# Kernel tuning notes

Measured on AMD Instinct MI355X. Metric: run time of the kernel, lower is better.

## Reference

```python
import jax, jax.numpy as jnp
import numpy as np

N_NODES = 50000
N_EDGES = 800000
D_IN = 256
HID = 128
OUT = 64
NEG_SLOPE = 0.2  # PyG GATConv default leaky_relu slope
EPS = 1e-16      # PyG softmax denominator epsilon


def _gat_conv(x, src, dst, W_src, W_dst, att_src, att_dst, bias, n_nodes):
    """Single-head PyG GATConv with add_self_loops=False.
    Returns (out [N, C_out], alpha [E])."""
    h_src = x @ W_src                     # [N, C]
    h_dst = x @ W_dst                     # [N, C]
    a_src = h_src @ att_src               # [N]
    a_dst = h_dst @ att_dst               # [N]
    logits = jax.nn.leaky_relu(a_src[src] + a_dst[dst], NEG_SLOPE)  # [E]
    # segment softmax over incoming edges of each dst node
    m = jax.ops.segment_max(logits, dst, num_segments=n_nodes)      # [N]
    e = jnp.exp(logits - m[dst])                                    # [E]
    denom = jax.ops.segment_sum(e, dst, num_segments=n_nodes)       # [N]
    alpha = e / (denom[dst] + EPS)                                  # [E]
    msg = h_src[src] * alpha[:, None]                               # [E, C]
    out = jax.ops.segment_sum(msg, dst, num_segments=n_nodes) + bias
    return out, alpha


def setup_inputs() -> dict:
    key = jax.random.key(0)
    ks = jax.random.split(key, 16)
    s = 0.05
    x = jax.random.normal(ks[0], (N_NODES, D_IN), dtype=jnp.float32)
    edge_index = jax.random.randint(ks[1], (2, N_EDGES), 0, N_NODES, dtype=jnp.int64)
    return {
        "x": x,
        "edge_index": edge_index,
        "W_src1": jax.random.normal(ks[2], (D_IN, HID), jnp.float32) * s,
        "W_dst1": jax.random.normal(ks[3], (D_IN, HID), jnp.float32) * s,
        "att_src1": jax.random.normal(ks[4], (HID,), jnp.float32) * s,
        "att_dst1": jax.random.normal(ks[5], (HID,), jnp.float32) * s,
        "b1": jnp.zeros((HID,), jnp.float32),
        "W_lin1": jax.random.normal(ks[6], (D_IN, HID), jnp.float32) * s,
        "b_lin1": jnp.zeros((HID,), jnp.float32),
        "W_src2": jax.random.normal(ks[7], (HID, OUT), jnp.float32) * s,
        "W_dst2": jax.random.normal(ks[8], (HID, OUT), jnp.float32) * s,
        "att_src2": jax.random.normal(ks[9], (OUT,), jnp.float32) * s,
        "att_dst2": jax.random.normal(ks[10], (OUT,), jnp.float32) * s,
        "b2": jnp.zeros((OUT,), jnp.float32),
        "W_lin2": jax.random.normal(ks[11], (HID, OUT), jnp.float32) * s,
        "b_lin2": jnp.zeros((OUT,), jnp.float32),
    }


def reference(x, edge_index, W_src1, W_dst1, att_src1, att_dst1, b1, W_lin1, b_lin1,
              W_src2, W_dst2, att_src2, att_dst2, b2, W_lin2, b_lin2):
    src, dst = edge_index[0], edge_index[1]
    n = x.shape[0]
    h, _ = _gat_conv(x, src, dst, W_src1, W_dst1, att_src1, att_dst1, b1, n)
    h = h + x @ W_lin1 + b_lin1
    h = jax.nn.relu(h)
    out, alpha = _gat_conv(h, src, dst, W_src2, W_dst2, att_src2, att_dst2, b2, n)
    out = out + h @ W_lin2 + b_lin2
    return out, alpha
```

## Files before the change

### kernel.cpp

```cpp
#include <hip/hip_runtime.h>
#include <math.h>

#define D_IN 256
#define HID 128
#define D_OUT 64
#define NEG_SLOPE 0.2f

#define NBUCK 392
#define BCAP  2560
#define P1_EPB 2048

typedef short short8 __attribute__((ext_vector_type(8)));
typedef float floatx4 __attribute__((ext_vector_type(4)));

__device__ __forceinline__ float wave_reduce_sum(float v) {
    #pragma unroll
    for (int off = 32; off > 0; off >>= 1) v += __shfl_xor(v, off, 64);
    return v;
}
__device__ __forceinline__ int wave_scan_incl_i(int v) {
    int lane = threadIdx.x & 63;
    #pragma unroll
    for (int off = 1; off < 64; off <<= 1) {
        int t = __shfl_up(v, off, 64);
        if (lane >= off) v += t;
    }
    return v;
}

__device__ __forceinline__ short f2bf(float f) {
    unsigned u = __float_as_uint(f);
    u += 0x7fffu + ((u >> 16) & 1u);
    return (short)(u >> 16);
}
__device__ __forceinline__ unsigned pk2(float a, float b) {
    return (unsigned)(unsigned short)f2bf(a) | ((unsigned)(unsigned short)f2bf(b) << 16);
}
__device__ __forceinline__ float bflo(unsigned p) { return __uint_as_float(p << 16); }
__device__ __forceinline__ float bfhi(unsigned p) { return __uint_as_float(p & 0xffff0000u); }

__global__ void prep_kernel(const float* __restrict__ Wsrc1, const float* __restrict__ att_src1,
                            const float* __restrict__ Wdst1, const float* __restrict__ att_dst1,
                            const float* __restrict__ Wsrc2, const float* __restrict__ att_src2,
                            const float* __restrict__ Wdst2, const float* __restrict__ att_dst2,
                            const float* __restrict__ b1, const float* __restrict__ b_lin1,
                            const float* __restrict__ b2, const float* __restrict__ b_lin2,
                            float* v_src1, float* v_dst1, float* v_src2, float* v_dst2,
                            float* bsum1, float* bsum2, int* bcur) {
    int t = threadIdx.x;
    if (t < D_IN) {
        float s1 = 0.f, s2 = 0.f;
        for (int c = 0; c < HID; c++) {
            s1 += Wsrc1[t * HID + c] * att_src1[c];
            s2 += Wdst1[t * HID + c] * att_dst1[c];
        }
        v_src1[t] = s1; v_dst1[t] = s2;
    }
    if (t < HID) {
        float s1 = 0.f, s2 = 0.f;
        for (int c = 0; c < D_OUT; c++) {
            s1 += Wsrc2[t * D_OUT + c] * att_src2[c];
            s2 += Wdst2[t * D_OUT + c] * att_dst2[c];
        }
        v_src2[t] = s1; v_dst2[t] = s2;
        bsum1[t] = b1[t] + b_lin1[t];
    }
    if (t < D_OUT) bsum2[t] = b2[t] + b_lin2[t];
    for (int i = t; i < NBUCK; i += 256) bcur[i] = 0;
}

__device__ void pack_body(const float* Wa, const float* Wb, short* Wp,
                          int NTG, int NH, int total, int idx) {
    if (idx >= total) return;
    int j = idx & 7;
    int lane = (idx >> 3) & 63;
    int r = idx >> 9;
    int nt = r % NTG;
    int s = r / NTG;
    int k = s * 32 + ((lane >> 4) * 8) + j;
    int cg = nt * 16 + (lane & 15);
    const float* W = (cg < NH) ? Wa : Wb;
    int col = (cg < NH) ? cg : cg - NH;
    Wp[idx] = f2bf(W[(size_t)k * NH + col]);
}

__device__ void bucket_scatter_body(const int* __restrict__ src, const int* __restrict__ dst,
                                    int E, int* bcur, unsigned* ebuf, int blk) {
    __shared__ int hist[NBUCK];
    __shared__ int gbase[NBUCK];
    int t = threadIdx.x;
    for (int i = t; i < NBUCK; i += 256) hist[i] = 0;
    __syncthreads();
    int e0 = blk * P1_EPB;
    int e1 = e0 + P1_EPB; if (e1 > E) e1 = E;
    for (int e = e0 + t; e < e1; e += 256)
        atomicAdd(&hist[dst[e] >> 7], 1);
    __syncthreads();
    for (int i = t; i < NBUCK; i += 256) {
        gbase[i] = atomicAdd(&bcur[i], hist[i]);
        hist[i] = 0;
    }
    __syncthreads();
    for (int e = e0 + t; e < e1; e += 256) {
        int d = dst[e];
        int b = d >> 7;
        int slot = atomicAdd(&hist[b], 1);
        int pos = gbase[b] + slot;
        if (pos < BCAP)
            ebuf[(size_t)b * BCAP + pos] = (unsigned)src[e] | ((unsigned)(d & 127) << 16);
    }
}

__device__ void convert_body(const float* __restrict__ X,
                             const float* __restrict__ vsrc, const float* __restrict__ vdst,
                             unsigned short* __restrict__ xb,
                             float* __restrict__ a_src, float* __restrict__ a_dst,
                             int Nn, int rb) {
    int row = rb * 4 + (threadIdx.x >> 6);
    int lane = threadIdx.x & 63;
    if (row >= Nn) return;
    float4 v = *(const float4*)(X + (size_t)row * D_IN + lane * 4);
    float4 vs = *(const float4*)(vsrc + lane * 4);
    float4 vd = *(const float4*)(vdst + lane * 4);
    float ps = v.x * vs.x + v.y * vs.y + v.z * vs.z + v.w * vs.w;
    float pd = v.x * vd.x + v.y * vd.y + v.z * vd.z + v.w * vd.w;
    ushort4 o;
    o.x = (unsigned short)f2bf(v.x); o.y = (unsigned short)f2bf(v.y);
    o.z = (unsigned short)f2bf(v.z); o.w = (unsigned short)f2bf(v.w);
    *(ushort4*)(xb + (size_t)row * D_IN + lane * 4) = o;
    ps = wave_reduce_sum(ps);
    pd = wave_reduce_sum(pd);
    if (lane == 0) { a_src[row] = ps; a_dst[row] = pd; }
}

__global__ void fused_pre(const int* __restrict__ src, const int* __restrict__ dst, int E,
                          int* bcur, unsigned* ebuf, int P1B,
                          const float* W_src1, const float* W_lin1, short* Wp1,
                          const float* W_src2, const float* W_lin2, short* Wp2,
                          const float* __restrict__ v_src1, const float* __restrict__ v_dst1,
                          float* a_src1, float* a_dst1,
                          const float* __restrict__ X, unsigned short* __restrict__ xb, int Nn) {
    int bid = blockIdx.x;
    if (bid < P1B) {
        bucket_scatter_body(src, dst, E, bcur, ebuf, bid);
    } else if (bid < P1B + 256) {
        pack_body(W_src1, W_lin1, Wp1, 16, HID, 8 * 16 * 512, (bid - P1B) * 256 + threadIdx.x);
    } else if (bid < P1B + 320) {
        pack_body(W_src2, W_lin2, Wp2, 8, D_OUT, 4 * 8 * 512, (bid - P1B - 256) * 256 + threadIdx.x);
    } else {
        convert_body(X, v_src1, v_dst1, xb, a_src1, a_dst1, Nn, bid - (P1B + 320));
    }
}

__device__ void build_csr_body(const int* __restrict__ bcur, const unsigned* __restrict__ ebuf,
                               int* __restrict__ ssrc, int* __restrict__ row_beg,
                               int* __restrict__ row_end, int Nn, int B) {
    __shared__ int cnt[128];
    __shared__ int ofs[128];
    __shared__ int wsum[2];
    int t = threadIdx.x;
    if (t < 128) cnt[t] = 0;
    __syncthreads();
    int n = bcur[B]; if (n > BCAP) n = BCAP;
    const unsigned* eb = ebuf + (size_t)B * BCAP;
    for (int i = t; i < n; i += 256)
        atomicAdd(&cnt[eb[i] >> 16], 1);
    __syncthreads();
    int base = B * BCAP;
    int v = 0, excl = 0;
    if (t < 128) {
        v = cnt[t];
        int incl = wave_scan_incl_i(v);
        if ((t & 63) == 63) wsum[t >> 6] = incl;
        excl = incl - v;
    }
    __syncthreads();
    if (t < 128) {
        if (t >= 64) excl += wsum[0];
        int node = B * 128 + t;
        if (node < Nn) { row_beg[node] = base + excl; row_end[node] = base + excl + v; }
        ofs[t] = base + excl;
    }
    __syncthreads();
    for (int i = t; i < n; i += 256) {
        unsigned r = eb[i];
        int pos = atomicAdd(&ofs[r >> 16], 1);
        ssrc[pos] = (int)(r & 0xffffu);
    }
}

template <int KS, int NT>
__device__ void gemm_body(const unsigned short* __restrict__ A,
                          const short* __restrict__ Wp,
                          const float* __restrict__ bias,
                          unsigned short* __restrict__ outb,
                          unsigned short* __restrict__ outc, int M, int bm) {
    const int K = KS * 32;
    const int NTG = 4 * NT;
    const int NH = NT * 32;
    int tid = threadIdx.x;
    int wave = tid >> 6, lane = tid & 63;
    int mr = lane & 15, quad = lane >> 4;

    floatx4 acc[4][NT];
    #pragma unroll
    for (int i = 0; i < 4; i++)
        #pragma unroll
        for (int j = 0; j < NT; j++) acc[i][j] = (floatx4){0.f, 0.f, 0.f, 0.f};

    const unsigned short* arow[4];
    #pragma unroll
    for (int tm = 0; tm < 4; tm++) {
        int gr = bm + tm * 16 + mr;
        if (gr >= M) gr = M - 1;
        arow[tm] = A + (size_t)gr * K + quad * 8;
    }
    const short* bbase = Wp + ((size_t)(wave * NT) * 64 + lane) * 8;

    #pragma unroll
    for (int s = 0; s < KS; s++) {
        short8 af[4], bf[NT];
        #pragma unroll
        for (int tm = 0; tm < 4; tm++)
            af[tm] = *(const short8*)(arow[tm] + s * 32);
        #pragma unroll
        for (int tn = 0; tn < NT; tn++)
            bf[tn] = *(const short8*)(bbase + ((size_t)s * NTG + tn) * 512);
        #pragma unroll
        for (int tn = 0; tn < NT; tn++)
            #pragma unroll
            for (int tm = 0; tm < 4; tm++)
                acc[tm][tn] = __builtin_amdgcn_mfma_f32_16x16x32_bf16(af[tm], bf[tn],
                                                                      acc[tm][tn], 0, 0, 0);
    }

    #pragma unroll
    for (int tm = 0; tm < 4; tm++) {
        #pragma unroll
        for (int tn = 0; tn < NT; tn++) {
            int cg = wave * NT * 16 + tn * 16 + mr;
            if (cg < NH) {
                #pragma unroll
                for (int r = 0; r < 4; r++) {
                    int gr = bm + tm * 16 + quad * 4 + r;
                    if (gr < M)
                        outb[(size_t)gr * NH + cg] = (unsigned short)f2bf(acc[tm][tn][r]);
                }
            } else {
                float bv = bias[cg - NH];
                #pragma unroll
                for (int r = 0; r < 4; r++) {
                    int gr = bm + tm * 16 + quad * 4 + r;
                    if (gr < M)
                        outc[(size_t)gr * NH + (cg - NH)] = (unsigned short)f2bf(acc[tm][tn][r] + bv);
                }
            }
        }
    }
}

__global__ __launch_bounds__(256, 3) void fused_g1(const unsigned short* __restrict__ xb,
                                                   const short* __restrict__ Wp1,
                                                   const float* __restrict__ bsum1,
                                                   unsigned short* __restrict__ h1b,
                                                   unsigned short* __restrict__ lin1b,
                                                   int M, int MB,
                                                   const int* __restrict__ bcur,
                                                   const unsigned* __restrict__ ebuf,
                                                   int* ssrc, int* row_beg, int* row_end, int Nn) {
    int bid = blockIdx.x;
    int c = bid >> 3, sub = bid & 7;
    int q = c / 3, r = c - q * 3;
    if (r == 2) {
        int B = q * 8 + sub;
        if (B < NBUCK)
            build_csr_body(bcur, ebuf, ssrc, row_beg, row_end, Nn, B);
    } else {
        int gb = (q * 2 + r) * 8 + sub;
        if (gb < MB)
            gemm_body<8, 4>(xb, Wp1, bsum1, h1b, lin1b, M, gb * 64);
    }
}

template <int KS, int NT>
__global__ __launch_bounds__(256, 3) void gemm_direct(const unsigned short* __restrict__ A,
                                                      const short* __restrict__ Wp,
                                                      const float* __restrict__ bias,
                                                      unsigned short* __restrict__ outb,
                                                      unsigned short* __restrict__ outc, int M) {
    gemm_body<KS, NT>(A, Wp, bias, outb, outc, M, blockIdx.x * 64);
}

__global__ void agg1_kernel(const int* __restrict__ row_beg, const int* __restrict__ row_end,
                            const int* __restrict__ ssrc,
                            const float* __restrict__ a_src, const float* __restrict__ a_dst,
                            const unsigned short* __restrict__ h1b,
                            const unsigned short* __restrict__ linb,
                            const float* __restrict__ vs2, const float* __restrict__ vd2,
                            unsigned short* __restrict__ hb,
                            float* __restrict__ a_src2, float* __restrict__ a_dst2, int Nn) {
    int node = blockIdx.x * 4 + (threadIdx.x >> 6);
    int lane = threadIdx.x & 63;
    if (node >= Nn) return;
    int beg = row_beg[node], end = row_end[node];
    float ad = a_dst[node];

    int qh = lane >> 4, cl = lane & 15;
    float acc[8] = {0.f, 0.f, 0.f, 0.f, 0.f, 0.f, 0.f, 0.f};
    float dsum = 0.f;
    const unsigned short* hcol = h1b + cl * 8;
    int j = beg + qh;
    for (; j + 4 < end; j += 8) {
        int s0 = ssrc[j], s1 = ssrc[j + 4];
        float l0 = a_src[s0] + ad; l0 = (l0 > 0.f) ? l0 : NEG_SLOPE * l0;
        float l1 = a_src[s1] + ad; l1 = (l1 > 0.f) ? l1 : NEG_SLOPE * l1;
        float w0 = __expf(l0), w1 = __expf(l1);
        uint4 p0 = *(const uint4*)(hcol + (size_t)s0 * HID);
        uint4 p1 = *(const uint4*)(hcol + (size_t)s1 * HID);
        acc[0] += w0 * bflo(p0.x); acc[1] += w0 * bfhi(p0.x);
        acc[2] += w0 * bflo(p0.y); acc[3] += w0 * bfhi(p0.y);
        acc[4] += w0 * bflo(p0.z); acc[5] += w0 * bfhi(p0.z);
        acc[6] += w0 * bflo(p0.w); acc[7] += w0 * bfhi(p0.w);
        acc[0] += w1 * bflo(p1.x); acc[1] += w1 * bfhi(p1.x);
        acc[2] += w1 * bflo(p1.y); acc[3] += w1 * bfhi(p1.y);
        acc[4] += w1 * bflo(p1.z); acc[5] += w1 * bfhi(p1.z);
        acc[6] += w1 * bflo(p1.w); acc[7] += w1 * bfhi(p1.w);
        if (cl == 0) dsum += w0 + w1;
    }
    for (; j < end; j += 4) {
        int s0 = ssrc[j];
        float l = a_src[s0] + ad; l = (l > 0.f) ? l : NEG_SLOPE * l;
        float w = __expf(l);
        uint4 p = *(const uint4*)(hcol + (size_t)s0 * HID);
        acc[0] += w * bflo(p.x); acc[1] += w * bfhi(p.x);
        acc[2] += w * bflo(p.y); acc[3] += w * bfhi(p.y);
        acc[4] += w * bflo(p.z); acc[5] += w * bfhi(p.z);
        acc[6] += w * bflo(p.w); acc[7] += w * bfhi(p.w);
        if (cl == 0) dsum += w;
    }
    #pragma unroll
    for (int i = 0; i < 8; i++) {
        acc[i] += __shfl_xor(acc[i], 16, 64);
        acc[i] += __shfl_xor(acc[i], 32, 64);
    }
    dsum = wave_reduce_sum(dsum);
    float inv = 1.f / (dsum + 1e-16f);

    int c = cl * 8;
    uint4 lb = *(const uint4*)(linb + (size_t)node * HID + c);
    float o[8];
    o[0] = fmaxf(acc[0] * inv + bflo(lb.x), 0.f);
    o[1] = fmaxf(acc[1] * inv + bfhi(lb.x), 0.f);
    o[2] = fmaxf(acc[2] * inv + bflo(lb.y), 0.f);
    o[3] = fmaxf(acc[3] * inv + bfhi(lb.y), 0.f);
    o[4] = fmaxf(acc[4] * inv + bflo(lb.z), 0.f);
    o[5] = fmaxf(acc[5] * inv + bfhi(lb.z), 0.f);
    o[6] = fmaxf(acc[6] * inv + bflo(lb.w), 0.f);
    o[7] = fmaxf(acc[7] * inv + bfhi(lb.w), 0.f);
    if (qh == 0) {
        uint4 pk;
        pk.x = pk2(o[0], o[1]); pk.y = pk2(o[2], o[3]);
        pk.z = pk2(o[4], o[5]); pk.w = pk2(o[6], o[7]);
        *(uint4*)&hb[(size_t)node * HID + c] = pk;
    }
    float ps = 0.f, pd = 0.f;
    #pragma unroll
    for (int i = 0; i < 8; i++) { ps += o[i] * vs2[c + i]; pd += o[i] * vd2[c + i]; }
    ps = wave_reduce_sum(ps) * 0.25f;
    pd = wave_reduce_sum(pd) * 0.25f;
    if (lane == 0) { a_src2[node] = ps; a_dst2[node] = pd; }
}

__global__ void agg2_kernel(const int* __restrict__ row_beg, const int* __restrict__ row_end,
                            const int* __restrict__ ssrc,
                            const float* __restrict__ a_src, const float* __restrict__ a_dst,
                            const unsigned short* __restrict__ h2b,
                            const unsigned short* __restrict__ lin2b,
                            float* __restrict__ out, float* __restrict__ sminv, int Nn) {
    int node = blockIdx.x * 4 + (threadIdx.x >> 6);
    int lane = threadIdx.x & 63;
    if (node >= Nn) return;
    int beg = row_beg[node], end = row_end[node];
    float ad = a_dst[node];

    int oh = lane >> 3, cl = lane & 7;
    float acc[8] = {0.f, 0.f, 0.f, 0.f, 0.f, 0.f, 0.f, 0.f};
    float dsum = 0.f;
    const unsigned short* hcol = h2b + cl * 8;
    int j = beg + oh;
    for (; j + 8 < end; j += 16) {
        int s0 = ssrc[j], s1 = ssrc[j + 8];
        float l0 = a_src[s0] + ad; l0 = (l0 > 0.f) ? l0 : NEG_SLOPE * l0;
        float l1 = a_src[s1] + ad; l1 = (l1 > 0.f) ? l1 : NEG_SLOPE * l1;
        float w0 = __expf(l0), w1 = __expf(l1);
        uint4 p0 = *(const uint4*)(hcol + (size_t)s0 * D_OUT);
        uint4 p1 = *(const uint4*)(hcol + (size_t)s1 * D_OUT);
        acc[0] += w0 * bflo(p0.x); acc[1] += w0 * bfhi(p0.x);
        acc[2] += w0 * bflo(p0.y); acc[3] += w0 * bfhi(p0.y);
        acc[4] += w0 * bflo(p0.z); acc[5] += w0 * bfhi(p0.z);
        acc[6] += w0 * bflo(p0.w); acc[7] += w0 * bfhi(p0.w);
        acc[0] += w1 * bflo(p1.x); acc[1] += w1 * bfhi(p1.x);
        acc[2] += w1 * bflo(p1.y); acc[3] += w1 * bfhi(p1.y);
        acc[4] += w1 * bflo(p1.z); acc[5] += w1 * bfhi(p1.z);
        acc[6] += w1 * bflo(p1.w); acc[7] += w1 * bfhi(p1.w);
        if (cl == 0) dsum += w0 + w1;
    }
    for (; j < end; j += 8) {
        int s0 = ssrc[j];
        float l = a_src[s0] + ad; l = (l > 0.f) ? l : NEG_SLOPE * l;
        float w = __expf(l);
        uint4 p = *(const uint4*)(hcol + (size_t)s0 * D_OUT);
        acc[0] += w * bflo(p.x); acc[1] += w * bfhi(p.x);
        acc[2] += w * bflo(p.y); acc[3] += w * bfhi(p.y);
        acc[4] += w * bflo(p.z); acc[5] += w * bfhi(p.z);
        acc[6] += w * bflo(p.w); acc[7] += w * bfhi(p.w);
        if (cl == 0) dsum += w;
    }
    #pragma unroll
    for (int i = 0; i < 8; i++) {
        acc[i] += __shfl_xor(acc[i], 8, 64);
        acc[i] += __shfl_xor(acc[i], 16, 64);
        acc[i] += __shfl_xor(acc[i], 32, 64);
    }
    dsum = wave_reduce_sum(dsum);
    float inv = 1.f / (dsum + 1e-16f);
    if (lane == 0) sminv[node] = inv;

    if (oh == 0) {
        int c = cl * 8;
        uint4 lb = *(const uint4*)(lin2b + (size_t)node * D_OUT + c);
        float4 oa = make_float4(acc[0] * inv + bflo(lb.x), acc[1] * inv + bfhi(lb.x),
                                acc[2] * inv + bflo(lb.y), acc[3] * inv + bfhi(lb.y));
        float4 ob = make_float4(acc[4] * inv + bflo(lb.z), acc[5] * inv + bfhi(lb.z),
                                acc[6] * inv + bflo(lb.w), acc[7] * inv + bfhi(lb.w));
        *(float4*)&out[(size_t)node * D_OUT + c] = oa;
        *(float4*)&out[(size_t)node * D_OUT + c + 4] = ob;
    }
}

__global__ void alpha_kernel(const int* __restrict__ src, const int* __restrict__ dst,
                             const float* __restrict__ a_src2, const float* __restrict__ a_dst2,
                             const float* __restrict__ sminv, float* __restrict__ alpha, int E) {
    int e = blockIdx.x * 256 + threadIdx.x;
    if (e >= E) return;
    int s = src[e], d = dst[e];
    float l = a_src2[s] + a_dst2[d];
    l = (l > 0.f) ? l : NEG_SLOPE * l;
    alpha[e] = __expf(l) * sminv[d];
}

extern "C" void kernel_launch(void* const* d_in, const int* in_sizes, int n_in,
                              void* d_out, int out_size, void* d_ws, size_t ws_size,
                              hipStream_t stream) {
    const float* x        = (const float*)d_in[0];
    const int*   ei       = (const int*)d_in[1];
    const float* W_src1   = (const float*)d_in[2];
    const float* W_dst1   = (const float*)d_in[3];
    const float* att_src1 = (const float*)d_in[4];
    const float* att_dst1 = (const float*)d_in[5];
    const float* b1       = (const float*)d_in[6];
    const float* W_lin1   = (const float*)d_in[7];
    const float* b_lin1   = (const float*)d_in[8];
    const float* W_src2   = (const float*)d_in[9];
    const float* W_dst2   = (const float*)d_in[10];
    const float* att_src2 = (const float*)d_in[11];
    const float* att_dst2 = (const float*)d_in[12];
    const float* b2       = (const float*)d_in[13];
    const float* W_lin2   = (const float*)d_in[14];
    const float* b_lin2   = (const float*)d_in[15];

    const int Nn = in_sizes[0] / D_IN;
    const int E  = in_sizes[1] / 2;
    const int* src = ei;
    const int* dst = ei + E;

    char* w = (char*)d_ws;
    auto alloc = [&](size_t bytes) { char* p = w; w += (bytes + 255) & ~(size_t)255; return p; };
    unsigned short* xb   = (unsigned short*)alloc((size_t)Nn * D_IN * 2);
    unsigned short* h1b  = (unsigned short*)alloc((size_t)Nn * HID * 2);
    unsigned short* lin1b= (unsigned short*)alloc((size_t)Nn * HID * 2);
    unsigned short* hb   = (unsigned short*)alloc((size_t)Nn * HID * 2);
    unsigned short* h2b  = (unsigned short*)alloc((size_t)Nn * D_OUT * 2);
    unsigned short* lin2b= (unsigned short*)alloc((size_t)Nn * D_OUT * 2);
    float* a_src1 = (float*)alloc((size_t)Nn * 4);
    float* a_dst1 = (float*)alloc((size_t)Nn * 4);
    float* a_src2 = (float*)alloc((size_t)Nn * 4);
    float* a_dst2 = (float*)alloc((size_t)Nn * 4);
    float* sminv  = (float*)alloc((size_t)Nn * 4);
    int*   row_beg= (int*)alloc((size_t)Nn * 4);
    int*   row_end= (int*)alloc((size_t)Nn * 4);
    int*   bcur   = (int*)alloc((size_t)NBUCK * 4);
    unsigned* ebuf= (unsigned*)alloc((size_t)NBUCK * BCAP * 4);
    int*   ssrc   = (int*)alloc((size_t)NBUCK * BCAP * 4);
    short* Wp1    = (short*)alloc((size_t)8 * 16 * 512 * 2);
    short* Wp2    = (short*)alloc((size_t)4 * 8 * 512 * 2);
    float* v_src1 = (float*)alloc(D_IN * 4);
    float* v_dst1 = (float*)alloc(D_IN * 4);
    float* v_src2 = (float*)alloc(HID * 4);
    float* v_dst2 = (float*)alloc(HID * 4);
    float* bsum1  = (float*)alloc(HID * 4);
    float* bsum2  = (float*)alloc(D_OUT * 4);

    float* out       = (float*)d_out;
    float* alpha_out = out + (size_t)Nn * D_OUT;

    prep_kernel<<<1, 256, 0, stream>>>(W_src1, att_src1, W_dst1, att_dst1,
                                       W_src2, att_src2, W_dst2, att_dst2,
                                       b1, b_lin1, b2, b_lin2,
                                       v_src1, v_dst1, v_src2, v_dst2, bsum1, bsum2, bcur);

    int P1B = (E + P1_EPB - 1) / P1_EPB;
    int ablocks = (Nn + 3) / 4;
    fused_pre<<<P1B + 320 + ablocks, 256, 0, stream>>>(src, dst, E, bcur, ebuf, P1B,
                                             W_src1, W_lin1, Wp1, W_src2, W_lin2, Wp2,
                                             v_src1, v_dst1, a_src1, a_dst1,
                                             x, xb, Nn);

    int mblocks = (Nn + 63) / 64;
    int gchunks = (mblocks + 7) / 8;
    int cchunks = (NBUCK + 7) / 8;
    int NI = (gchunks + cchunks) * 8;
    fused_g1<<<NI, 256, 0, stream>>>(xb, Wp1, bsum1, h1b, lin1b, Nn,
                                     mblocks, bcur, ebuf, ssrc, row_beg, row_end, Nn);

    agg1_kernel<<<ablocks, 256, 0, stream>>>(row_beg, row_end, ssrc, a_src1, a_dst1, h1b, lin1b,
                                             v_src2, v_dst2, hb, a_src2, a_dst2, Nn);

    gemm_direct<4, 2><<<mblocks, 256, 0, stream>>>(hb, Wp2, bsum2, h2b, lin2b, Nn);
    agg2_kernel<<<ablocks, 256, 0, stream>>>(row_beg, row_end, ssrc, a_src2, a_dst2, h2b, lin2b,
                                             out, sminv, Nn);
    int eblocks = (E + 255) / 256;
    alpha_kernel<<<eblocks, 256, 0, stream>>>(src, dst, a_src2, a_dst2, sminv, alpha_out, E);
}
```

Before: 276.9 us.

## Split aggregation kernels across feature column slices and parallelize prep kernel

The agg1 and agg2 kernels now give each node's feature columns to 4 and 2 blocks respectively. Each wave processes 16 edges in parallel with 4 lanes per 32-column slice, instead of spreading lanes over all columns. This raises edge-level parallelism and the number of blocks for the gather-heavy aggregation. The cost is recomputing edge weights, softmax denominators and index loads once per slice. Partial a_src2/a_dst2 dot products are accumulated with atomics into buffers zeroed by memsets, and prep_kernel is spread across 25 blocks with shuffle reductions.

Result: slower. 361.5 us (+30.5%).

```diff
diff --git a/kernel.cpp b/kernel.cpp
--- a/kernel.cpp
+++ b/kernel.cpp
@@ -47,26 +47,42 @@
                             const float* __restrict__ b2, const float* __restrict__ b_lin2,
                             float* v_src1, float* v_dst1, float* v_src2, float* v_dst2,
                             float* bsum1, float* bsum2, int* bcur) {
-    int t = threadIdx.x;
-    if (t < D_IN) {
+    int bid = blockIdx.x, t = threadIdx.x;
+    if (bid < 16) {
+        int r = bid * 16 + (t >> 4), sub = t & 15;
         float s1 = 0.f, s2 = 0.f;
-        for (int c = 0; c < HID; c++) {
-            s1 += Wsrc1[t * HID + c] * att_src1[c];
-            s2 += Wdst1[t * HID + c] * att_dst1[c];
+        #pragma unroll
+        for (int k = 0; k < 8; k++) {
+            int c = sub * 8 + k;
+            s1 += Wsrc1[r * HID + c] * att_src1[c];
+            s2 += Wdst1[r * HID + c] * att_dst1[c];
         }
-        v_src1[t] = s1; v_dst1[t] = s2;
-    }
-    if (t < HID) {
+        #pragma unroll
+        for (int off = 8; off > 0; off >>= 1) {
+            s1 += __shfl_xor(s1, off, 16);
+            s2 += __shfl_xor(s2, off, 16);
+        }
+        if (sub == 0) { v_src1[r] = s1; v_dst1[r] = s2; }
+    } else if (bid < 24) {
+        int r = (bid - 16) * 16 + (t >> 4), sub = t & 15;
         float s1 = 0.f, s2 = 0.f;
-        for (int c = 0; c < D_OUT; c++) {
-            s1 += Wsrc2[t * D_OUT + c] * att_src2[c];
-            s2 += Wdst2[t * D_OUT + c] * att_dst2[c];
+        #pragma unroll
+        for (int k = 0; k < 4; k++) {
+            int c = sub * 4 + k;
+            s1 += Wsrc2[r * D_OUT + c] * att_src2[c];
+            s2 += Wdst2[r * D_OUT + c] * att_dst2[c];
         }
-        v_src2[t] = s1; v_dst2[t] = s2;
-        bsum1[t] = b1[t] + b_lin1[t];
-    }
-    if (t < D_OUT) bsum2[t] = b2[t] + b_lin2[t];
-    for (int i = t; i < NBUCK; i += 256) bcur[i] = 0;
+        #pragma unroll
+        for (int off = 8; off > 0; off >>= 1) {
+            s1 += __shfl_xor(s1, off, 16);
+            s2 += __shfl_xor(s2, off, 16);
+        }
+        if (sub == 0) { v_src2[r] = s1; v_dst2[r] = s2; }
+    } else {
+        if (t < HID) bsum1[t] = b1[t] + b_lin1[t];
+        if (t < D_OUT) bsum2[t] = b2[t] + b_lin2[t];
+        for (int i = t; i < NBUCK; i += 256) bcur[i] = 0;
+    }
 }
 
 __device__ void pack_body(const float* Wa, const float* Wb, short* Wp,
@@ -299,54 +315,39 @@
                             const float* __restrict__ vs2, const float* __restrict__ vd2,
                             unsigned short* __restrict__ hb,
                             float* __restrict__ a_src2, float* __restrict__ a_dst2, int Nn) {
-    int node = blockIdx.x * 4 + (threadIdx.x >> 6);
+    int q = blockIdx.x & 3;
+    int node = (blockIdx.x >> 2) * 4 + (threadIdx.x >> 6);
     int lane = threadIdx.x & 63;
     if (node >= Nn) return;
     int beg = row_beg[node], end = row_end[node];
     float ad = a_dst[node];
 
-    int qh = lane >> 4, cl = lane & 15;
+    int eslot = lane >> 2, cg = lane & 3;
+    int c = q * 32 + cg * 8;
+    const unsigned short* hcol = h1b + c;
     float acc[8] = {0.f, 0.f, 0.f, 0.f, 0.f, 0.f, 0.f, 0.f};
     float dsum = 0.f;
-    const unsigned short* hcol = h1b + cl * 8;
-    int j = beg + qh;
-    for (; j + 4 < end; j += 8) {
-        int s0 = ssrc[j], s1 = ssrc[j + 4];
-        float l0 = a_src[s0] + ad; l0 = (l0 > 0.f) ? l0 : NEG_SLOPE * l0;
-        float l1 = a_src[s1] + ad; l1 = (l1 > 0.f) ? l1 : NEG_SLOPE * l1;
-        float w0 = __expf(l0), w1 = __expf(l1);
-        uint4 p0 = *(const uint4*)(hcol + (size_t)s0 * HID);
-        uint4 p1 = *(const uint4*)(hcol + (size_t)s1 * HID);
-        acc[0] += w0 * bflo(p0.x); acc[1] += w0 * bfhi(p0.x);
-        acc[2] += w0 * bflo(p0.y); acc[3] += w0 * bfhi(p0.y);
-        acc[4] += w0 * bflo(p0.z); acc[5] += w0 * bfhi(p0.z);
-        acc[6] += w0 * bflo(p0.w); acc[7] += w0 * bfhi(p0.w);
-        acc[0] += w1 * bflo(p1.x); acc[1] += w1 * bfhi(p1.x);
-        acc[2] += w1 * bflo(p1.y); acc[3] += w1 * bfhi(p1.y);
-        acc[4] += w1 * bflo(p1.z); acc[5] += w1 * bfhi(p1.z);
-        acc[6] += w1 * bflo(p1.w); acc[7] += w1 * bfhi(p1.w);
-        if (cl == 0) dsum += w0 + w1;
-    }
-    for (; j < end; j += 4) {
-        int s0 = ssrc[j];
-        float l = a_src[s0] + ad; l = (l > 0.f) ? l : NEG_SLOPE * l;
+    for (int j = beg + eslot; j < end; j += 16) {
+        int s = ssrc[j];
+        float l = a_src[s] + ad; l = (l > 0.f) ? l : NEG_SLOPE * l;
         float w = __expf(l);
-        uint4 p = *(const uint4*)(hcol + (size_t)s0 * HID);
+        uint4 p = *(const uint4*)(hcol + (size_t)s * HID);
         acc[0] += w * bflo(p.x); acc[1] += w * bfhi(p.x);
         acc[2] += w * bflo(p.y); acc[3] += w * bfhi(p.y);
         acc[4] += w * bflo(p.z); acc[5] += w * bfhi(p.z);
         acc[6] += w * bflo(p.w); acc[7] += w * bfhi(p.w);
-        if (cl == 0) dsum += w;
+        if (cg == 0) dsum += w;
     }
     #pragma unroll
     for (int i = 0; i < 8; i++) {
+        acc[i] += __shfl_xor(acc[i], 4, 64);
+        acc[i] += __shfl_xor(acc[i], 8, 64);
         acc[i] += __shfl_xor(acc[i], 16, 64);
         acc[i] += __shfl_xor(acc[i], 32, 64);
     }
     dsum = wave_reduce_sum(dsum);
     float inv = 1.f / (dsum + 1e-16f);
 
-    int c = cl * 8;
     uint4 lb = *(const uint4*)(linb + (size_t)node * HID + c);
     float o[8];
     o[0] = fmaxf(acc[0] * inv + bflo(lb.x), 0.f);
@@ -357,7 +358,7 @@
     o[5] = fmaxf(acc[5] * inv + bfhi(lb.z), 0.f);
     o[6] = fmaxf(acc[6] * inv + bflo(lb.w), 0.f);
     o[7] = fmaxf(acc[7] * inv + bfhi(lb.w), 0.f);
-    if (qh == 0) {
+    if (eslot == 0) {
         uint4 pk;
         pk.x = pk2(o[0], o[1]); pk.y = pk2(o[2], o[3]);
         pk.z = pk2(o[4], o[5]); pk.w = pk2(o[6], o[7]);
@@ -366,9 +367,12 @@
     float ps = 0.f, pd = 0.f;
     #pragma unroll
     for (int i = 0; i < 8; i++) { ps += o[i] * vs2[c + i]; pd += o[i] * vd2[c + i]; }
-    ps = wave_reduce_sum(ps) * 0.25f;
-    pd = wave_reduce_sum(pd) * 0.25f;
-    if (lane == 0) { a_src2[node] = ps; a_dst2[node] = pd; }
+    ps = wave_reduce_sum(ps) * 0.0625f;
+    pd = wave_reduce_sum(pd) * 0.0625f;
+    if (lane == 0) {
+        atomicAdd(&a_src2[node], ps);
+        atomicAdd(&a_dst2[node], pd);
+    }
 }
 
 __global__ void agg2_kernel(const int* __restrict__ row_beg, const int* __restrict__ row_end,
@@ -377,57 +381,41 @@
                             const unsigned short* __restrict__ h2b,
                             const unsigned short* __restrict__ lin2b,
                             float* __restrict__ out, float* __restrict__ sminv, int Nn) {
-    int node = blockIdx.x * 4 + (threadIdx.x >> 6);
+    int h = blockIdx.x & 1;
+    int node = (blockIdx.x >> 1) * 4 + (threadIdx.x >> 6);
     int lane = threadIdx.x & 63;
     if (node >= Nn) return;
     int beg = row_beg[node], end = row_end[node];
     float ad = a_dst[node];
 
-    int oh = lane >> 3, cl = lane & 7;
+    int eslot = lane >> 2, cg = lane & 3;
+    int c = h * 32 + cg * 8;
+    const unsigned short* hcol = h2b + c;
     float acc[8] = {0.f, 0.f, 0.f, 0.f, 0.f, 0.f, 0.f, 0.f};
     float dsum = 0.f;
-    const unsigned short* hcol = h2b + cl * 8;
-    int j = beg + oh;
-    for (; j + 8 < end; j += 16) {
-        int s0 = ssrc[j], s1 = ssrc[j + 8];
-        float l0 = a_src[s0] + ad; l0 = (l0 > 0.f) ? l0 : NEG_SLOPE * l0;
-        float l1 = a_src[s1] + ad; l1 = (l1 > 0.f) ? l1 : NEG_SLOPE * l1;
-        float w0 = __expf(l0), w1 = __expf(l1);
-        uint4 p0 = *(const uint4*)(hcol + (size_t)s0 * D_OUT);
-        uint4 p1 = *(const uint4*)(hcol + (size_t)s1 * D_OUT);
-        acc[0] += w0 * bflo(p0.x); acc[1] += w0 * bfhi(p0.x);
-        acc[2] += w0 * bflo(p0.y); acc[3] += w0 * bfhi(p0.y);
-        acc[4] += w0 * bflo(p0.z); acc[5] += w0 * bfhi(p0.z);
-        acc[6] += w0 * bflo(p0.w); acc[7] += w0 * bfhi(p0.w);
-        acc[0] += w1 * bflo(p1.x); acc[1] += w1 * bfhi(p1.x);
-        acc[2] += w1 * bflo(p1.y); acc[3] += w1 * bfhi(p1.y);
-        acc[4] += w1 * bflo(p1.z); acc[5] += w1 * bfhi(p1.z);
-        acc[6] += w1 * bflo(p1.w); acc[7] += w1 * bfhi(p1.w);
-        if (cl == 0) dsum += w0 + w1;
-    }
-    for (; j < end; j += 8) {
-        int s0 = ssrc[j];
-        float l = a_src[s0] + ad; l = (l > 0.f) ? l : NEG_SLOPE * l;
+    for (int j = beg + eslot; j < end; j += 16) {
+        int s = ssrc[j];
+        float l = a_src[s] + ad; l = (l > 0.f) ? l : NEG_SLOPE * l;
         float w = __expf(l);
-        uint4 p = *(const uint4*)(hcol + (size_t)s0 * D_OUT);
+        uint4 p = *(const uint4*)(hcol + (size_t)s * D_OUT);
         acc[0] += w * bflo(p.x); acc[1] += w * bfhi(p.x);
         acc[2] += w * bflo(p.y); acc[3] += w * bfhi(p.y);
         acc[4] += w * bflo(p.z); acc[5] += w * bfhi(p.z);
         acc[6] += w * bflo(p.w); acc[7] += w * bfhi(p.w);
-        if (cl == 0) dsum += w;
+        if (cg == 0) dsum += w;
     }
     #pragma unroll
     for (int i = 0; i < 8; i++) {
+        acc[i] += __shfl_xor(acc[i], 4, 64);
         acc[i] += __shfl_xor(acc[i], 8, 64);
         acc[i] += __shfl_xor(acc[i], 16, 64);
         acc[i] += __shfl_xor(acc[i], 32, 64);
     }
     dsum = wave_reduce_sum(dsum);
     float inv = 1.f / (dsum + 1e-16f);
-    if (lane == 0) sminv[node] = inv;
-
-    if (oh == 0) {
-        int c = cl * 8;
+    if (h == 0 && lane == 0) sminv[node] = inv;
+
+    if (eslot == 0) {
         uint4 lb = *(const uint4*)(lin2b + (size_t)node * D_OUT + c);
         float4 oa = make_float4(acc[0] * inv + bflo(lb.x), acc[1] * inv + bfhi(lb.x),
                                 acc[2] * inv + bflo(lb.y), acc[3] * inv + bfhi(lb.y));
@@ -504,10 +492,13 @@
     float* out       = (float*)d_out;
     float* alpha_out = out + (size_t)Nn * D_OUT;
 
-    prep_kernel<<<1, 256, 0, stream>>>(W_src1, att_src1, W_dst1, att_dst1,
-                                       W_src2, att_src2, W_dst2, att_dst2,
-                                       b1, b_lin1, b2, b_lin2,
-                                       v_src1, v_dst1, v_src2, v_dst2, bsum1, bsum2, bcur);
+    hipMemsetAsync(a_src2, 0, (size_t)Nn * 4, stream);
+    hipMemsetAsync(a_dst2, 0, (size_t)Nn * 4, stream);
+
+    prep_kernel<<<25, 256, 0, stream>>>(W_src1, att_src1, W_dst1, att_dst1,
+                                        W_src2, att_src2, W_dst2, att_dst2,
+                                        b1, b_lin1, b2, b_lin2,
+                                        v_src1, v_dst1, v_src2, v_dst2, bsum1, bsum2, bcur);
 
     int P1B = (E + P1_EPB - 1) / P1_EPB;
     int ablocks = (Nn + 3) / 4;
@@ -523,12 +514,13 @@
     fused_g1<<<NI, 256, 0, stream>>>(xb, Wp1, bsum1, h1b, lin1b, Nn,
                                      mblocks, bcur, ebuf, ssrc, row_beg, row_end, Nn);
 
-    agg1_kernel<<<ablocks, 256, 0, stream>>>(row_beg, row_end, ssrc, a_src1, a_dst1, h1b, lin1b,
-                                             v_src2, v_dst2, hb, a_src2, a_dst2, Nn);
+    agg1_kernel<<<ablocks * 4, 256, 0, stream>>>(row_beg, row_end, ssrc, a_src1, a_dst1,
+                                                 h1b, lin1b, v_src2, v_dst2, hb,
+                                                 a_src2, a_dst2, Nn);
 
     gemm_direct<4, 2><<<mblocks, 256, 0, stream>>>(hb, Wp2, bsum2, h2b, lin2b, Nn);
-    agg2_kernel<<<ablocks, 256, 0, stream>>>(row_beg, row_end, ssrc, a_src2, a_dst2, h2b, lin2b,
-                                             out, sminv, Nn);
+    agg2_kernel<<<ablocks * 2, 256, 0, stream>>>(row_beg, row_end, ssrc, a_src2, a_dst2,
+                                                 h2b, lin2b, out, sminv, Nn);
     int eblocks = (E + 255) / 256;
     alpha_kernel<<<eblocks, 256, 0, stream>>>(src, dst, a_src2, a_dst2, sminv, alpha_out, E);
 }
```
